# Performance work log

Measured on AMD Instinct MI355X. Metric: run time of the kernel, lower is better.

## Reference

```python
import jax, jax.numpy as jnp
import numpy as np
from jax import lax
from jax.scipy.special import logsumexp

TRIGGER_SIZE = 34
NTAG = TRIGGER_SIZE + 2  # +START/STOP
START = TRIGGER_SIZE
STOP = TRIGGER_SIZE + 1


def setup_inputs() -> dict:
    key = jax.random.key(0)
    k1, k2, k3, k4, k5 = jax.random.split(key, 5)
    B, S, H = 64, 512, 768
    x_1 = jax.random.normal(k1, (B, S, H), dtype=jnp.float32)
    head_indexes = jax.random.randint(k2, (B, S), 0, S)
    triggers_y = jax.random.randint(k3, (B, S), 0, TRIGGER_SIZE)
    W = jax.random.normal(k4, (H, NTAG), dtype=jnp.float32) * (1.0 / np.sqrt(H))
    b = jnp.zeros((NTAG,), dtype=jnp.float32)
    transitions = jax.random.normal(k5, (NTAG, NTAG), dtype=jnp.float32) * 0.1
    return {"x_1": x_1, "head_indexes": head_indexes, "triggers_y": triggers_y,
            "W": W, "b": b, "transitions": transitions}


def crf_nll(emit, mask, tags, trans):
    # emit [B,S,T], mask [B,S] bool, tags [B,S], trans [T,T] (from->to)
    B, S, T = emit.shape
    maskf = mask.astype(emit.dtype)
    # --- partition (forward algorithm) ---
    alpha0 = emit[:, 0] + trans[START][None, :]  # [B,T]; pos 0 always valid

    def fstep(alpha, inp):
        e_t, m_t = inp  # [B,T], [B]
        new = logsumexp(alpha[:, :, None] + trans[None, :, :], axis=1) + e_t
        return jnp.where(m_t[:, None], new, alpha), None

    alpha, _ = lax.scan(fstep, alpha0,
                        (emit[:, 1:].transpose(1, 0, 2), mask[:, 1:].T))
    logZ = logsumexp(alpha + trans[:, STOP][None, :], axis=1)  # [B]
    # --- gold path score ---
    emit_g = jnp.take_along_axis(emit, tags[:, :, None], axis=2)[..., 0]  # [B,S]
    emit_score = (emit_g * maskf).sum(axis=1)
    trans_pair = trans[tags[:, :-1], tags[:, 1:]]  # [B,S-1]
    trans_score = (trans_pair * maskf[:, 1:]).sum(axis=1)
    xlen = mask.sum(axis=1)  # [B]
    last_tag = jnp.take_along_axis(tags, (xlen - 1)[:, None], axis=1)[:, 0]
    gold = emit_score + trans[START, tags[:, 0]] + trans_score + trans[last_tag, STOP]
    return jnp.sum(logZ - gold)


def crf_viterbi(emit, mask, trans):
    B, S, T = emit.shape
    ids = jnp.arange(T)
    delta0 = emit[:, 0] + trans[START][None, :]

    def vstep(delta, inp):
        e_t, m_t = inp
        scores = delta[:, :, None] + trans[None, :, :]  # [B,T,T]
        best = scores.max(axis=1) + e_t
        bp = jnp.argmax(scores, axis=1)  # [B,T]
        new_delta = jnp.where(m_t[:, None], best, delta)
        bp = jnp.where(m_t[:, None], bp, ids[None, :])  # identity on pad
        return new_delta, bp

    delta, bps = lax.scan(vstep, delta0,
                          (emit[:, 1:].transpose(1, 0, 2), mask[:, 1:].T))
    final = delta + trans[:, STOP][None, :]
    last_tag = jnp.argmax(final, axis=1)  # [B]
    path_score = jnp.max(final, axis=1)

    def back(tag_next, bp_t):
        tag_t = jnp.take_along_axis(bp_t, tag_next[:, None], axis=1)[:, 0]
        return tag_t, tag_t

    _, prev_tags = lax.scan(back, last_tag, bps, reverse=True)  # [S-1,B]
    path = jnp.concatenate([prev_tags.T, last_tag[:, None]], axis=1)  # [B,S]
    path = jnp.where(mask, path, 0)
    return path_score, path


def reference(x_1, head_indexes, triggers_y, W, b, transitions):
    B, S, H = x_1.shape
    # batched version of the per-sample index_select loop
    x = jnp.take_along_axis(x_1, head_indexes[:, :, None], axis=1)  # [B,S,H]
    xlen = head_indexes.max(axis=1)  # xlen = [max(row) for row in head_indexes]
    mask = jnp.arange(S)[None, :] < xlen[:, None]  # [B,S] bool
    logits = jax.nn.leaky_relu(x @ W + b)  # tri_fc1 + leaky_relu (dropout=eval)
    trigger_loss = crf_nll(logits, mask, triggers_y, transitions)
    path_score, trigger_hat = crf_viterbi(logits, mask, transitions)
    return trigger_loss, trigger_hat, path_score
```

## Files before the change

kernel.cpp:

```cpp
#include <hip/hip_runtime.h>
#include <math.h>

#define SB 64
#define SS 512
#define SH 768
#define NT 36
#define TSTART 34
#define TSTOP 35
#define NC 32
#define CL 16

#define CFENCE() asm volatile("" ::: "memory")

__device__ __forceinline__ float wave_max_f(float v) {
#pragma unroll
    for (int off = 32; off > 0; off >>= 1) v = fmaxf(v, __shfl_xor(v, off, 64));
    return v;
}
__device__ __forceinline__ float wave_sum_f(float v) {
#pragma unroll
    for (int off = 32; off > 0; off >>= 1) v += __shfl_xor(v, off, 64);
    return v;
}
__device__ __forceinline__ float bcast0(float v) {
    return __uint_as_float(__builtin_amdgcn_readfirstlane(__float_as_uint(v)));
}

#define DOT4(pv, k4)                                                     \
    {                                                                    \
        const float* wr = Wq + (size_t)((k4) * 4) * NT;                  \
        _Pragma("unroll")                                                \
        for (int j = 0; j < NT; ++j) acc[j] += (pv).x * wr[j];           \
        _Pragma("unroll")                                                \
        for (int j = 0; j < NT; ++j) acc[j] += (pv).y * wr[NT + j];      \
        _Pragma("unroll")                                                \
        for (int j = 0; j < NT; ++j) acc[j] += (pv).z * wr[2 * NT + j];  \
        _Pragma("unroll")                                                \
        for (int j = 0; j < NT; ++j) acc[j] += (pv).w * wr[3 * NT + j];  \
    }

extern "C" __global__ __launch_bounds__(512) void k_emit(
    const float* __restrict__ x1, const int* __restrict__ hidx,
    const float* __restrict__ W, const float* __restrict__ bias,
    float* __restrict__ emit)
{
    __shared__ __align__(16) float red[8][64][37];

    int tid  = threadIdx.x;
    int lane = tid & 63;
    int q    = __builtin_amdgcn_readfirstlane(tid >> 6);
    int gr   = blockIdx.x * 64 + lane;
    int b    = gr >> 9;
    const float4* xr = (const float4*)(x1 + (size_t)(b * SS + hidx[gr]) * SH) + q * 24;
    const float*  Wq = W + (size_t)q * 96 * NT;

    float acc[NT];
#pragma unroll
    for (int j = 0; j < NT; ++j) acc[j] = 0.f;

    float4 p0 = xr[0], p1 = xr[1], p2 = xr[2], p3 = xr[3];
    for (int kb = 0; kb < 20; kb += 4) {
        float4 n0 = xr[kb + 4];
        float4 n1 = xr[kb + 5];
        float4 n2 = xr[kb + 6];
        float4 n3 = xr[kb + 7];
        DOT4(p0, kb);
        DOT4(p1, kb + 1);
        DOT4(p2, kb + 2);
        DOT4(p3, kb + 3);
        p0 = n0; p1 = n1; p2 = n2; p3 = n3;
    }
    DOT4(p0, 20);
    DOT4(p1, 21);
    DOT4(p2, 22);
    DOT4(p3, 23);

#pragma unroll
    for (int j = 0; j < NT; ++j) red[q][lane][j] = acc[j];
    __syncthreads();

    int r = tid >> 2, g = tid & 3;
    float vout[9];
    if (tid < 256) {
#pragma unroll
        for (int jj = 0; jj < 9; ++jj) {
            int j = g * 9 + jj;
            float v = bias[j];
#pragma unroll
            for (int qq = 0; qq < 8; ++qq) v += red[qq][r][j];
            vout[jj] = v > 0.f ? v : 0.01f * v;
        }
    }
    __syncthreads();
    if (tid < 256) {
        float* st = &red[0][0][0];
#pragma unroll
        for (int jj = 0; jj < 9; ++jj) st[r * NT + g * 9 + jj] = vout[jj];
    }
    __syncthreads();
    {
        const float4* st4 = (const float4*)&red[0][0][0];
        float4* op = (float4*)(emit + (size_t)blockIdx.x * 64 * NT);
        for (int i = tid; i < 576; i += 512) op[i] = st4[i];
    }
}

#define LSE_STEP(T)                                                       \
    {                                                                     \
        float e_t = elsw[((T) - t0s) * NT + jj];                          \
        float m = bcast0(alpha);                                          \
        float p = __expf(alpha - m);                                      \
        bc[lane] = p;                                                     \
        CFENCE();                                                         \
        __builtin_amdgcn_wave_barrier();                                  \
        float s0 = 0.f, s1 = 0.f, s2 = 0.f, s3 = 0.f;                     \
        _Pragma("unroll")                                                 \
        for (int k = 0; k < 9; ++k) {                                     \
            float4 pv = bc4[w][k];                                        \
            s0 += pv.x * Ecol[4 * k];                                     \
            s1 += pv.y * Ecol[4 * k + 1];                                 \
            s2 += pv.z * Ecol[4 * k + 2];                                 \
            s3 += pv.w * Ecol[4 * k + 3];                                 \
        }                                                                 \
        CFENCE();                                                         \
        float anew = m + __logf((s0 + s1) + (s2 + s3)) + e_t;             \
        alpha = act ? anew : -1e30f;                                      \
    }

#define VIT_STEP(T, WRITEBP)                                              \
    {                                                                     \
        float e_t = elsw[((T) - t0s) * NT + jj];                          \
        bc[lane] = alpha;                                                 \
        CFENCE();                                                         \
        __builtin_amdgcn_wave_barrier();                                  \
        float b0 = -1e30f, b1 = -1e30f, b2 = -1e30f, b3 = -1e30f;         \
        int   i0 = 0, i1 = 1, i2 = 2, i3 = 3;                             \
        _Pragma("unroll")                                                 \
        for (int k = 0; k < 9; ++k) {                                     \
            float4 dv = bc4[w][k];                                        \
            float c0 = dv.x + tcol[4 * k];                                 \
            float c1 = dv.y + tcol[4 * k + 1];                             \
            float c2 = dv.z + tcol[4 * k + 2];                             \
            float c3 = dv.w + tcol[4 * k + 3];                             \
            if (c0 > b0) { b0 = c0; i0 = 4 * k; }                         \
            if (c1 > b1) { b1 = c1; i1 = 4 * k + 1; }                     \
            if (c2 > b2) { b2 = c2; i2 = 4 * k + 2; }                     \
            if (c3 > b3) { b3 = c3; i3 = 4 * k + 3; }                     \
        }                                                                 \
        CFENCE();                                                         \
        float best = b0; int bi = i0;                                     \
        if (b1 > best || (b1 == best && i1 < bi)) { best = b1; bi = i1; } \
        if (b2 > best || (b2 == best && i2 < bi)) { best = b2; bi = i2; } \
        if (b3 > best || (b3 == best && i3 < bi)) { best = b3; bi = i3; } \
        float dnew = best + e_t;                                          \
        alpha = act ? dnew : -1e30f;                                      \
        if ((WRITEBP) && act)                                             \
            bp[((size_t)b * SS + (T)) * 64 + jj] = (unsigned char)bi;     \
    }

extern "C" __global__ __launch_bounds__(256) void k_scan(
    const float* __restrict__ emit, const int* __restrict__ hidx,
    const float* __restrict__ trans,
    float* __restrict__ Warr, float* __restrict__ Earr,
    float* __restrict__ lse_local,
    float* __restrict__ score_local, int* __restrict__ ltag,
    unsigned char* __restrict__ bp)
{
    __shared__ float trl[NT * NT];
    __shared__ float els[4][1024];
    __shared__ float4 bc4[4][16];

    int tid  = threadIdx.x;
    int lane = tid & 63;
    int w    = __builtin_amdgcn_readfirstlane(tid >> 6);

    int wid  = blockIdx.x * 4 + w;
    int kind = wid >> 11;
    int rem  = wid & 2047;
    int b    = rem >> 5;
    int c    = rem & 31;

    const float* eb  = emit + (size_t)b * SS * NT;
    int t0s = (c > 0) ? (c * CL - 9) : 0;
    const float* ebase = eb + (size_t)t0s * NT;
    float* elsw = els[w];

#pragma unroll
    for (int i = 0; i < 4; ++i) {
        __builtin_amdgcn_global_load_lds(
            (const __attribute__((address_space(1))) void*)(ebase + i * 256 + lane * 4),
            (__attribute__((address_space(3))) void*)(elsw + i * 256), 16, 0, 0);
    }
    for (int i = tid; i < NT * NT; i += 256) trl[i] = trans[i];

    int  jj  = lane < NT ? lane : NT - 1;
    bool act = lane < NT;

    int xm = 0;
    const int* hb = hidx + b * SS;
#pragma unroll
    for (int k = 0; k < SS / 64; ++k) xm = max(xm, hb[lane + 64 * k]);
#pragma unroll
    for (int off = 32; off > 0; off >>= 1) xm = max(xm, __shfl_xor(xm, off, 64));
    int xlen = xm;
    int cl   = (xlen >= 1) ? ((xlen - 1) >> 4) : 0;

    int tb0 = c * CL - 8;
    int te0 = c * CL; if (te0 > xlen) te0 = xlen; te0 -= 1;
    int tb  = c * CL; if (tb < 1) tb = 1;
    int te  = (c + 1) * CL; if (te > xlen) te = xlen; te -= 1;

    int didx = (kind * SB + b) * NC + c;

    float alpha;
    if (c == 0) alpha = act ? (eb[jj] + trans[TSTART * NT + jj]) : -1e30f;
    else        alpha = act ? eb[(size_t)(tb0 - 1) * NT + jj] : -1e30f;

    __syncthreads();

    float* bc = (float*)bc4[w];

    if (kind == 0) {
        float Ecol[NT];
#pragma unroll
        for (int i = 0; i < NT; ++i) Ecol[i] = __expf(trl[i * NT + jj]);
        if (c > 0) {
            for (int t = tb0; t <= te0; ++t) LSE_STEP(t)
        }
        float Wv = bcast0(alpha);
        for (int t = tb; t <= te; ++t) LSE_STEP(t)
        float Ev = bcast0(alpha);
        if (lane == 0) { Warr[didx] = Wv; Earr[didx] = Ev; }
        if (c == cl) {
            float ff = act ? (alpha + trl[jj * NT + TSTOP]) : -1e30f;
            float M = wave_max_f(ff);
            float ssum = wave_sum_f(__expf(ff - M));
            if (lane == 0) lse_local[b] = M + __logf(ssum);
        }
    } else {
        float tcol[NT];
#pragma unroll
        for (int i = 0; i < NT; ++i) tcol[i] = trl[i * NT + jj];
        if (c > 0) {
            for (int t = tb0; t <= te0; ++t) VIT_STEP(t, 0)
        }
        float Wv = bcast0(alpha);
        for (int t = tb; t <= te; ++t) VIT_STEP(t, 1)
        float Ev = bcast0(alpha);
        if (lane == 0) { Warr[didx] = Wv; Earr[didx] = Ev; }
        if (c == cl) {
            float ff = act ? (alpha + trl[jj * NT + TSTOP]) : -1e30f;
            float bv = ff; int bi = lane;
#pragma unroll
            for (int off = 32; off > 0; off >>= 1) {
                float ov = __shfl_xor(bv, off, 64);
                int   oi = __shfl_xor(bi, off, 64);
                if (ov > bv || (ov == bv && oi < bi)) { bv = ov; bi = oi; }
            }
            if (lane == 0) { score_local[b] = bv; ltag[b] = bi; }
        }
    }
}

extern "C" __global__ __launch_bounds__(1024) void k_final(
    const float* __restrict__ emit, const int* __restrict__ hidx,
    const int* __restrict__ tags, const float* __restrict__ trans,
    const float* __restrict__ Warr, const float* __restrict__ Earr,
    const float* __restrict__ lse_local,
    const float* __restrict__ score_local, const int* __restrict__ ltag,
    const unsigned char* __restrict__ bp,
    float* __restrict__ loss_out, float* __restrict__ path_out,
    float* __restrict__ score_out)
{
    __shared__ unsigned char bpl[SS * 64];
    __shared__ unsigned char cmap[SS][40];
    __shared__ unsigned char exitmap[NC][64];
    __shared__ float gred[16];
    __shared__ int   ent[NC];

    int tid  = threadIdx.x;
    int lane = tid & 63;
    int w    = tid >> 6;
    int b    = blockIdx.x;

    {
        const int4* src = (const int4*)(bp + (size_t)b * SS * 64);
        int4* dst = (int4*)bpl;
        for (int i = tid; i < SS * 4; i += 1024) dst[i] = src[i];
    }

    int xm = 0;
    const int* hb = hidx + b * SS;
#pragma unroll
    for (int k = 0; k < SS / 64; ++k) xm = max(xm, hb[lane + 64 * k]);
#pragma unroll
    for (int off = 32; off > 0; off >>= 1) xm = max(xm, __shfl_xor(xm, off, 64));
    int xlen = xm;
    int cl   = (xlen >= 1) ? ((xlen - 1) >> 4) : 0;

    float g = 0.f;
    const int* tg = tags + b * SS;
    if (tid < SS) {
        int t = tid;
        if (t < xlen) {
            int tt = tg[t];
            g += emit[((size_t)b * SS + t) * NT + tt];
            if (t >= 1) g += trans[tg[t - 1] * NT + tt];
        }
    }
    g = wave_sum_f(g);
    if (lane == 0) gred[w] = g;

    float kf = 0.f, kv = 0.f;
    if (w == 8) {
        if (lane < cl) {
            kf = Earr[(0 * SB + b) * NC + lane] - Warr[(0 * SB + b) * NC + lane + 1];
            kv = Earr[(1 * SB + b) * NC + lane] - Warr[(1 * SB + b) * NC + lane + 1];
        }
        kf = wave_sum_f(kf);
        kv = wave_sum_f(kv);
    }

    __syncthreads();

    if (tid == 512) {
        float gold = 0.f;
#pragma unroll
        for (int i = 0; i < 8; ++i) gold += gred[i];
        int tg0 = tg[0];
        int lt  = (xlen >= 1) ? tg[xlen - 1] : tg0;
        gold += trans[TSTART * NT + tg0] + trans[lt * NT + TSTOP];
        atomicAdd(loss_out, (lse_local[b] + kf) - gold);
        score_out[b] = score_local[b] + kv;
    }

    for (int cc = 0; cc < 2; ++cc) {
        int c = w * 2 + cc;
        if (xlen >= 1 && c <= cl) {
            int tb = (c == 0) ? 1 : c * CL;
            int te = c * CL + CL - 1; if (te > xlen - 1) te = xlen - 1;
            int m = lane;
            if (lane < NT) cmap[te][lane] = (unsigned char)m;
            for (int t = te; t >= tb; --t) {
                m = bpl[t * 64 + m];
                if (lane < NT) {
                    if (t > tb || c == 0) cmap[t - 1][lane] = (unsigned char)m;
                    else                  exitmap[c][lane]  = (unsigned char)m;
                }
            }
        }
    }
    __syncthreads();

    if (tid == 0 && xlen >= 1) {
        int e = ltag[b];
        for (int c2 = cl; c2 >= 0; --c2) {
            ent[c2] = e;
            if (c2 > 0) e = exitmap[c2][e];
        }
    }
    __syncthreads();

    if (tid < SS) {
        int t = tid;
        float* op = path_out + (size_t)b * SS;
        if (t >= xlen) op[t] = 0.f;
        else           op[t] = (float)cmap[t][ent[t >> 4]];
    }
}

extern "C" void kernel_launch(void* const* d_in, const int* in_sizes, int n_in,
                              void* d_out, int out_size, void* d_ws, size_t ws_size,
                              hipStream_t stream)
{
    const float* x1    = (const float*)d_in[0];
    const int*   hidx  = (const int*)d_in[1];
    const int*   tags  = (const int*)d_in[2];
    const float* W     = (const float*)d_in[3];
    const float* bias  = (const float*)d_in[4];
    const float* trans = (const float*)d_in[5];
    float* out = (float*)d_out;

    float* emit        = (float*)d_ws;
    float* Warr        = emit + (size_t)SB * SS * NT;
    float* Earr        = Warr + 2 * SB * NC;
    float* lse_local   = Earr + 2 * SB * NC;
    float* score_local = lse_local + SB;
    int*   ltag        = (int*)(score_local + SB);
    float* spacer      = (float*)(ltag + SB);
    unsigned char* bp  = (unsigned char*)(spacer + SB);

    hipLaunchKernelGGL(k_emit, dim3(SB * SS / 64), dim3(512), 0, stream,
                       x1, hidx, W, bias, emit);
    hipLaunchKernelGGL(k_scan, dim3(1024), dim3(256), 0, stream,
                       emit, hidx, trans, Warr, Earr, lse_local,
                       score_local, ltag, bp);
    hipLaunchKernelGGL(k_final, dim3(SB), dim3(1024), 0, stream,
                       emit, hidx, tags, trans, Warr, Earr, lse_local,
                       score_local, ltag, bp, out, out + 1, out + 1 + SB * SS);
}
```

Baseline: 202.0 us.

## Stage gathered x rows through double-buffered LDS with coalesced row loads

The emission GEMV kernel no longer has each lane read its own strided 96-float slice of a gathered row. Eight threads now cooperatively load each row with coalesced float4 reads into a padded, double-buffered shared-memory tile, and compute waves read from that tile in 128-column chunks. This is meant to improve global-load coalescing for the row gather and to overlap loads with FMAs. In exchange it adds six block-wide barriers and more LDS traffic, and LDS grows to about 75 KB, which may limit occupancy.

```diff
diff --git a/kernel.cpp b/kernel.cpp
--- a/kernel.cpp
+++ b/kernel.cpp
@@ -26,57 +26,74 @@
     return __uint_as_float(__builtin_amdgcn_readfirstlane(__float_as_uint(v)));
 }
 
-#define DOT4(pv, k4)                                                     \
-    {                                                                    \
-        const float* wr = Wq + (size_t)((k4) * 4) * NT;                  \
-        _Pragma("unroll")                                                \
-        for (int j = 0; j < NT; ++j) acc[j] += (pv).x * wr[j];           \
-        _Pragma("unroll")                                                \
-        for (int j = 0; j < NT; ++j) acc[j] += (pv).y * wr[NT + j];      \
-        _Pragma("unroll")                                                \
-        for (int j = 0; j < NT; ++j) acc[j] += (pv).z * wr[2 * NT + j];  \
-        _Pragma("unroll")                                                \
-        for (int j = 0; j < NT; ++j) acc[j] += (pv).w * wr[3 * NT + j];  \
-    }
+#define XP 129
+#define XBUF 8256
+#define RED(qq, rr, jj) smem[(qq) * 2368 + (rr) * 37 + (jj)]
 
 extern "C" __global__ __launch_bounds__(512) void k_emit(
     const float* __restrict__ x1, const int* __restrict__ hidx,
     const float* __restrict__ W, const float* __restrict__ bias,
     float* __restrict__ emit)
 {
-    __shared__ __align__(16) float red[8][64][37];
+    __shared__ __align__(16) float smem[18944];
 
     int tid  = threadIdx.x;
     int lane = tid & 63;
     int q    = __builtin_amdgcn_readfirstlane(tid >> 6);
-    int gr   = blockIdx.x * 64 + lane;
-    int b    = gr >> 9;
-    const float4* xr = (const float4*)(x1 + (size_t)(b * SS + hidx[gr]) * SH) + q * 24;
-    const float*  Wq = W + (size_t)q * 96 * NT;
+
+    int srow = tid >> 3;
+    int c8   = tid & 7;
+    int grs  = blockIdx.x * 64 + srow;
+    int bs   = grs >> 9;
+    const float4* srcRow = (const float4*)(x1 + (size_t)(bs * SS + hidx[grs]) * SH);
+    int woff = srow * XP + c8 * 4;
 
     float acc[NT];
 #pragma unroll
     for (int j = 0; j < NT; ++j) acc[j] = 0.f;
 
-    float4 p0 = xr[0], p1 = xr[1], p2 = xr[2], p3 = xr[3];
-    for (int kb = 0; kb < 20; kb += 4) {
-        float4 n0 = xr[kb + 4];
-        float4 n1 = xr[kb + 5];
-        float4 n2 = xr[kb + 6];
-        float4 n3 = xr[kb + 7];
-        DOT4(p0, kb);
-        DOT4(p1, kb + 1);
-        DOT4(p2, kb + 2);
-        DOT4(p3, kb + 3);
-        p0 = n0; p1 = n1; p2 = n2; p3 = n3;
-    }
-    DOT4(p0, 20);
-    DOT4(p1, 21);
-    DOT4(p2, 22);
-    DOT4(p3, 23);
-
-#pragma unroll
-    for (int j = 0; j < NT; ++j) red[q][lane][j] = acc[j];
+    float4 n0, n1, n2, n3;
+    n0 = srcRow[c8];  n1 = srcRow[c8 + 8];
+    n2 = srcRow[c8 + 16]; n3 = srcRow[c8 + 24];
+    {
+        float* d = smem + woff;
+        d[0] = n0.x; d[1] = n0.y; d[2] = n0.z; d[3] = n0.w;
+        d[32] = n1.x; d[33] = n1.y; d[34] = n1.z; d[35] = n1.w;
+        d[64] = n2.x; d[65] = n2.y; d[66] = n2.z; d[67] = n2.w;
+        d[96] = n3.x; d[97] = n3.y; d[98] = n3.z; d[99] = n3.w;
+    }
+
+#pragma unroll
+    for (int s = 0; s < 6; ++s) {
+        if (s < 5) {
+            int f0 = (s + 1) * 32 + c8;
+            n0 = srcRow[f0]; n1 = srcRow[f0 + 8];
+            n2 = srcRow[f0 + 16]; n3 = srcRow[f0 + 24];
+        }
+        __syncthreads();
+        {
+            const float* xs = smem + (s & 1) * XBUF + lane * XP + 16 * q;
+            const float* Ws = W + (size_t)(128 * s + 16 * q) * NT;
+#pragma unroll
+            for (int k = 0; k < 16; ++k) {
+                float xv = xs[k];
+                const float* wr = Ws + k * NT;
+#pragma unroll
+                for (int j = 0; j < NT; ++j) acc[j] += xv * wr[j];
+            }
+        }
+        if (s < 5) {
+            float* d = smem + ((s + 1) & 1) * XBUF + woff;
+            d[0] = n0.x; d[1] = n0.y; d[2] = n0.z; d[3] = n0.w;
+            d[32] = n1.x; d[33] = n1.y; d[34] = n1.z; d[35] = n1.w;
+            d[64] = n2.x; d[65] = n2.y; d[66] = n2.z; d[67] = n2.w;
+            d[96] = n3.x; d[97] = n3.y; d[98] = n3.z; d[99] = n3.w;
+        }
+    }
+    __syncthreads();
+
+#pragma unroll
+    for (int j = 0; j < NT; ++j) RED(q, lane, j) = acc[j];
     __syncthreads();
 
     int r = tid >> 2, g = tid & 3;
@@ -87,19 +104,18 @@
             int j = g * 9 + jj;
             float v = bias[j];
 #pragma unroll
-            for (int qq = 0; qq < 8; ++qq) v += red[qq][r][j];
+            for (int qq = 0; qq < 8; ++qq) v += RED(qq, r, j);
             vout[jj] = v > 0.f ? v : 0.01f * v;
         }
     }
     __syncthreads();
     if (tid < 256) {
-        float* st = &red[0][0][0];
-#pragma unroll
-        for (int jj = 0; jj < 9; ++jj) st[r * NT + g * 9 + jj] = vout[jj];
+#pragma unroll
+        for (int jj = 0; jj < 9; ++jj) smem[r * NT + g * 9 + jj] = vout[jj];
     }
     __syncthreads();
     {
-        const float4* st4 = (const float4*)&red[0][0][0];
+        const float4* st4 = (const float4*)smem;
         float4* op = (float4*)(emit + (size_t)blockIdx.x * 64 * NT);
         for (int i = tid; i < 576; i += 512) op[i] = st4[i];
     }
```

After: 220.2 us. 1.09x slower.
